# Performance work log

Measured on AMD Instinct MI355X. Metric: run time of the kernel, lower is better.

The kernel has to match this reference:

```python
import jax, jax.numpy as jnp
import numpy as np

EPS = 1e-7
MAX_TAN_NORM = 10.0  # safe_expmap0 clamp


def logmap0(x):
    # x: [..., D] Lorentz point, x[..., 0] = time component (>= 1)
    x0 = x[..., :1]
    xs = x[..., 1:]
    d = jnp.arccosh(jnp.clip(x0, 1.0 + EPS, None))          # geodesic distance to origin
    ns = jnp.clip(jnp.linalg.norm(xs, axis=-1, keepdims=True), EPS, None)
    return jnp.concatenate([jnp.zeros_like(x0), d * xs / ns], axis=-1)


def safe_expmap0(u):
    # u: tangent at origin; time component is projected out (proju at origin)
    us = u[..., 1:]
    n = jnp.clip(jnp.linalg.norm(us, axis=-1, keepdims=True), EPS, None)
    nc = jnp.minimum(n, MAX_TAN_NORM)                        # clamp norm for stability
    usc = us * (nc / n)
    return jnp.concatenate([jnp.cosh(nc), jnp.sinh(nc) * usc / nc], axis=-1)


def projx(x):
    # re-project onto the hyperboloid: x0 = sqrt(1 + ||xs||^2)
    xs = x[..., 1:]
    x0 = jnp.sqrt(1.0 + jnp.sum(xs * xs, axis=-1, keepdims=True))
    return jnp.concatenate([x0, xs], axis=-1)


def lorentz_linear(x_hyp, W, b):
    t = logmap0(x_hyp)
    y = t @ W.T + b
    return projx(safe_expmap0(y))


def setup_inputs() -> dict:
    key = jax.random.key(0)
    ks = jax.random.split(key, 8)
    N, D_IN, D_HID, D_OUT = 8192, 1024, 4096, 1024
    s = 0.02
    x_sp = jax.random.normal(ks[0], (N, D_IN), dtype=jnp.float32)
    x_hyp = projx(x_sp)  # valid Lorentz point (time comp overwritten)
    W1 = jax.random.normal(ks[1], (D_HID, D_IN), dtype=jnp.float32) * s
    b1 = jnp.zeros((D_HID,), dtype=jnp.float32)
    W2 = jax.random.normal(ks[2], (D_HID, D_HID), dtype=jnp.float32) * s
    b2 = jnp.zeros((D_HID,), dtype=jnp.float32)
    W3 = jax.random.normal(ks[3], (D_OUT, D_HID), dtype=jnp.float32) * s
    b3 = jnp.zeros((D_OUT,), dtype=jnp.float32)
    return {"x_hyp": x_hyp, "W1": W1, "b1": b1, "W2": W2, "b2": b2, "W3": W3, "b3": b3}


def reference(x_hyp, W1, b1, W2, b2, W3, b3):
    # layers[:-1] with inter-layer logmap0 -> (dropout=identity in eval) -> expmap0 -> projx
    h = lorentz_linear(x_hyp, W1, b1)
    h = projx(safe_expmap0(logmap0(h)))
    h = lorentz_linear(h, W2, b2)
    h = projx(safe_expmap0(logmap0(h)))
    return lorentz_linear(h, W3, b3)
```

## Files before the change

### kernel.cpp

```cpp
#include <hip/hip_runtime.h>
#include <stdint.h>

#define EPSF 1e-7f
#define MAXTAN 10.0f

typedef __bf16 bf16x8 __attribute__((ext_vector_type(8)));
typedef float floatx4 __attribute__((ext_vector_type(4)));
typedef __attribute__((address_space(3))) void lds_void_t;
typedef __attribute__((address_space(1))) void gbl_void_t;

__device__ __forceinline__ unsigned short f2bf(float x) {
  union { float f; uint32_t u; } v; v.f = x;
  uint32_t u = v.u;
  u += 0x7fffu + ((u >> 16) & 1u);
  return (unsigned short)(u >> 16);
}
__device__ __forceinline__ float bf2f(unsigned short h) {
  union { uint32_t u; float f; } v; v.u = ((uint32_t)h) << 16;
  return v.f;
}

__device__ __forceinline__ int sniff_mode(const unsigned short* x) {
  int sane = 0;
  for (int i = 0; i < 128; ++i) {
    unsigned short h = x[i];
    int e = (h >> 7) & 0xFF;
    if ((h & 0x7FFF) == 0 || (e >= 96 && e <= 140)) ++sane;
  }
  return (sane >= 120) ? 1 : 0;
}

__global__ void k_init(const unsigned short* __restrict__ x, int* __restrict__ modeg,
                       const void* __restrict__ b1, const void* __restrict__ b2,
                       const void* __restrict__ b3, float* __restrict__ o1,
                       float* __restrict__ o2, float* __restrict__ o3) {
  __shared__ int mds;
  if (threadIdx.x == 0) {
    int m = sniff_mode(x);
    mds = m;
    if (blockIdx.x == 0) *modeg = m;
  }
  __syncthreads();
  int m = mds;
  int i = blockIdx.x * 256 + threadIdx.x;
  if (i < 4096) o1[i] = m ? bf2f(((const unsigned short*)b1)[i]) : ((const float*)b1)[i];
  if (i < 4096) o2[i] = m ? bf2f(((const unsigned short*)b2)[i]) : ((const float*)b2)[i];
  if (i < 1024) o3[i] = m ? bf2f(((const unsigned short*)b3)[i]) : ((const float*)b3)[i];
}

__global__ void k_prep(const void* __restrict__ xv, unsigned short* __restrict__ xb,
                       float* __restrict__ sc0, float* __restrict__ x0c,
                       const int* __restrict__ mode) {
  const int row = blockIdx.x;
  const int tid = threadIdx.x;
  float4 v;
  if (*mode) {
    ushort4 u = ((const ushort4*)((const unsigned short*)xv + (size_t)row * 1024))[tid];
    v.x = bf2f(u.x); v.y = bf2f(u.y); v.z = bf2f(u.z); v.w = bf2f(u.w);
  } else {
    v = ((const float4*)((const float*)xv + (size_t)row * 1024))[tid];
  }
  ushort4 o;
  o.x = f2bf(v.x); o.y = f2bf(v.y); o.z = f2bf(v.z); o.w = f2bf(v.w);
  ((ushort4*)(xb + (size_t)row * 1024))[tid] = o;

  float s = v.x * v.x + v.y * v.y + v.z * v.z + v.w * v.w;
  if (tid == 0) s -= v.x * v.x;
  for (int off = 32; off; off >>= 1) s += __shfl_down(s, off, 64);
  __shared__ float red[4];
  if ((tid & 63) == 0) red[tid >> 6] = s;
  __syncthreads();
  if (tid == 0) {
    s = red[0] + red[1] + red[2] + red[3];
    float ns = fmaxf(sqrtf(s), EPSF);
    float d = acoshf(fmaxf(v.x, 1.0f + EPSF));
    sc0[row] = d / ns;
    x0c[row] = bf2f(o.x);
  }
}

template<int K8>
__global__ void k_cvtw(const void* __restrict__ in, unsigned short* __restrict__ out,
                       const int* __restrict__ mode, int n8, float* __restrict__ c0) {
  int i = blockIdx.x * 256 + threadIdx.x;
  if (i >= n8) return;
  if (*mode) {
    uint4 g = ((const uint4*)in)[i];
    ((uint4*)out)[i] = g;
    if (i % K8 == 0) c0[i / K8] = bf2f((unsigned short)(g.x & 0xFFFFu));
  } else {
    float4 a = ((const float4*)in)[2 * i];
    float4 b = ((const float4*)in)[2 * i + 1];
    ushort4 oa, ob;
    oa.x = f2bf(a.x); oa.y = f2bf(a.y); oa.z = f2bf(a.z); oa.w = f2bf(a.w);
    ob.x = f2bf(b.x); ob.y = f2bf(b.y); ob.z = f2bf(b.z); ob.w = f2bf(b.w);
    ((ushort4*)out)[2 * i] = oa;
    ((ushort4*)out)[2 * i + 1] = ob;
    if (i % K8 == 0) c0[i / K8] = bf2f(oa.x);
  }
}

template<int NBLK>
__global__ void k_sc(const float* __restrict__ part, const unsigned short* __restrict__ y,
                     int stride, float* __restrict__ sc, float* __restrict__ c0,
                     float* __restrict__ ssout, int nrows) {
  int i = blockIdx.x * 256 + threadIdx.x;
  if (i >= nrows) return;
  float s = 0.f;
#pragma unroll
  for (int j = 0; j < NBLK; ++j) s += part[(size_t)i * NBLK + j];
  float n = fmaxf(sqrtf(fmaxf(s, 0.f)), EPSF);
  sc[i] = fminf(n, MAXTAN) / n;
  c0[i] = bf2f(y[(size_t)i * stride]);
  if (ssout) ssout[i] = s;
}

__global__ void k_final(const unsigned short* __restrict__ y, const float* __restrict__ ss,
                        void* __restrict__ outv, const int* __restrict__ mode) {
  const int row = blockIdx.x;
  const int tid = threadIdx.x;
  float n = fmaxf(sqrtf(fmaxf(ss[row], 0.f)), EPSF);
  float nc = fminf(n, MAXTAN);
  float a = sinhf(nc) / n;
  ushort4 u = ((const ushort4*)(y + (size_t)row * 1024))[tid];
  float4 o;
  o.x = bf2f(u.x) * a; o.y = bf2f(u.y) * a;
  o.z = bf2f(u.z) * a; o.w = bf2f(u.w) * a;
  if (tid == 0) o.x = coshf(nc);
  if (*mode) {
    ushort4 o16;
    o16.x = f2bf(o.x); o16.y = f2bf(o.y); o16.z = f2bf(o.z); o16.w = f2bf(o.w);
    ((ushort4*)outv)[(size_t)row * 256 + tid] = o16;
  } else {
    ((float4*)outv)[(size_t)row * 256 + tid] = o;
  }
}

template<int N, int K, int NBLK, int GX>
__global__ __launch_bounds__(256, 4) void k_gemm_bt(
    const unsigned short* __restrict__ A,
    const unsigned short* __restrict__ B,
    const float* __restrict__ bias,
    const float* __restrict__ sc,
    const float* __restrict__ c0f,
    const float* __restrict__ wc0,
    unsigned short* __restrict__ Cb,
    float* __restrict__ part)
{
  __shared__ __align__(16) unsigned short As[128 * 32];
  __shared__ __align__(16) unsigned short Bs[128 * 32];

  const int tid  = threadIdx.x;
  const int wave = tid >> 6;
  const int lane = tid & 63;
  const int quad = lane >> 4;
  const int m16  = lane & 15;

  const int j = blockIdx.x & 7;
  const int k = blockIdx.x >> 3;
  int bxi, byi;
  if (GX == 32) {
    bxi = 16 * (j & 1) + (k & 15);
    byi = 16 * (j >> 1) + (k >> 4);
  } else {
    bxi = k & 7;
    byi = 8 * j + (k >> 3);
  }
  const int bm = byi * 128;
  const int bn = bxi * 128;

  const int srow = lane >> 2;
  const int scol = (((lane & 3) ^ ((srow >> 1) & 3)) << 3);

  const int wm = (wave >> 1) << 6;
  const int wn = (wave & 1) << 6;

  const int rsw = ((quad ^ ((m16 >> 1) & 3)) << 3);

  const int c0i = wave * 2;
  const unsigned short* ga0 = A + (size_t)(bm + c0i * 16 + srow) * K + scol;
  const unsigned short* ga1 = ga0 + (size_t)16 * K;
  const unsigned short* gb0 = B + (size_t)(bn + c0i * 16 + srow) * K + scol;
  const unsigned short* gb1 = gb0 + (size_t)16 * K;

  floatx4 acc[4][4];
#pragma unroll
  for (int i = 0; i < 4; ++i)
#pragma unroll
    for (int jj = 0; jj < 4; ++jj)
#pragma unroll
      for (int r = 0; r < 4; ++r) acc[i][jj][r] = 0.0f;

  for (int k0 = 0; k0 < K; k0 += 32) {
    __builtin_amdgcn_global_load_lds((gbl_void_t*)(void*)ga0,
                                     (lds_void_t*)(As + c0i * 512), 16, 0, 0);
    __builtin_amdgcn_global_load_lds((gbl_void_t*)(void*)ga1,
                                     (lds_void_t*)(As + c0i * 512 + 512), 16, 0, 0);
    __builtin_amdgcn_global_load_lds((gbl_void_t*)(void*)gb0,
                                     (lds_void_t*)(Bs + c0i * 512), 16, 0, 0);
    __builtin_amdgcn_global_load_lds((gbl_void_t*)(void*)gb1,
                                     (lds_void_t*)(Bs + c0i * 512 + 512), 16, 0, 0);
    ga0 += 32; ga1 += 32; gb0 += 32; gb1 += 32;
    __syncthreads();

    bf16x8 af[4], bfg[4];
#pragma unroll
    for (int t = 0; t < 4; ++t) {
      af[t]  = *(const bf16x8*)(As + (wm + t * 16 + m16) * 32 + rsw);
      bfg[t] = *(const bf16x8*)(Bs + (wn + t * 16 + m16) * 32 + rsw);
    }
#pragma unroll
    for (int mt = 0; mt < 4; ++mt)
#pragma unroll
      for (int nt = 0; nt < 4; ++nt)
        acc[mt][nt] = __builtin_amdgcn_mfma_f32_16x16x32_bf16(af[mt], bfg[nt], acc[mt][nt], 0, 0, 0);
    __syncthreads();
  }

#pragma unroll
  for (int mt = 0; mt < 4; ++mt) {
#pragma unroll
    for (int r = 0; r < 4; ++r) {
      const int gm = bm + wm + mt * 16 + quad * 4 + r;
      const float scv = sc[gm];
      const float c0v = c0f[gm];
      float sq = 0.f;
#pragma unroll
      for (int nt = 0; nt < 4; ++nt) {
        const int gn = bn + wn + nt * 16 + m16;
        float v = scv * (acc[mt][nt][r] - c0v * wc0[gn]) + bias[gn];
        Cb[(size_t)gm * N + gn] = f2bf(v);
        sq += (gn == 0) ? 0.f : v * v;
      }
      sq += __shfl_xor(sq, 1, 64);
      sq += __shfl_xor(sq, 2, 64);
      sq += __shfl_xor(sq, 4, 64);
      sq += __shfl_xor(sq, 8, 64);
      if (m16 == 0) part[(size_t)gm * NBLK + 2 * bxi + (wave & 1)] = sq;
    }
  }
}

template<int N, int K>
__global__ __launch_bounds__(512, 2) void k_gemm256(
    const unsigned short* __restrict__ A,
    const unsigned short* __restrict__ B,
    const float* __restrict__ bias,
    const float* __restrict__ sc,
    const float* __restrict__ c0f,
    const float* __restrict__ wc0,
    unsigned short* __restrict__ Cb,
    float* __restrict__ part)
{
  static_assert(K % 128 == 0 && K / 32 >= 8, "need NT multiple of 4, >= 8");
  constexpr int NT = K / 32;
  __shared__ __align__(16) unsigned short S[4][2][8192];

  const int tid  = threadIdx.x;
  const int wave = tid >> 6;
  const int lane = tid & 63;
  const int quad = lane >> 4;
  const int m16  = lane & 15;
  const int wr   = wave >> 2;
  const int wc   = wave & 3;

  const int j = blockIdx.x & 7;
  const int k = blockIdx.x >> 3;
  const int bxi = 8 * (j & 1) + (k & 7);
  const int byi = 8 * (j >> 1) + (k >> 3);
  const int bm = byi * 256;
  const int bn = bxi * 256;

  const int gsw8 = (((tid & 3) ^ ((tid >> 3) & 3)) << 3);
  const unsigned short* gAp = A + (size_t)(bm + (tid >> 2)) * K + gsw8;
  const unsigned short* gAq = gAp + (size_t)128 * K;
  const unsigned short* gBp = B + (size_t)(bn + (tid >> 2)) * K + gsw8;
  const unsigned short* gBq = gBp + (size_t)128 * K;
  const int ldw = wave * 1024;

  const int rsw8 = ((quad ^ ((m16 >> 1) & 3)) << 3);
  const int aoffB = ((wr * 128 + m16) * 32 + rsw8) * 2;
  const int boffB = ((wc * 64  + m16) * 32 + rsw8) * 2;
  const char* Sb  = (const char*)&S[0][0][0];
  const char* pA  = Sb + aoffB;
  const char* pA2 = pA + 65536;
  const char* pB  = Sb + 16384 + boffB;
  const char* pB2 = pB + 65536;

  floatx4 acc[8][4];
#pragma unroll
  for (int i = 0; i < 8; ++i)
#pragma unroll
    for (int jj = 0; jj < 4; ++jj)
#pragma unroll
      for (int r = 0; r < 4; ++r) acc[i][jj][r] = 0.0f;

#define GLL(SRC, DST) __builtin_amdgcn_global_load_lds((gbl_void_t*)(void*)(SRC), (lds_void_t*)(DST), 16, 0, 0)
#define ARD(S_, M_) (*(const bf16x8*)(((S_) < 2 ? pA : pA2) + ((S_) * 32768 + (M_) * 1024 - ((S_) < 2 ? 0 : 65536))))
#define BRD(S_, N_) (*(const bf16x8*)(((S_) < 2 ? pB : pB2) + ((S_) * 32768 + (N_) * 1024 - ((S_) < 2 ? 0 : 65536))))
#define STG(T_, OFF) { \
    GLL(gAp + (OFF), (char*)Sb + (T_) * 32768 +         ldw); \
    GLL(gAq + (OFF), (char*)Sb + (T_) * 32768 +  8192 + ldw); \
    GLL(gBp + (OFF), (char*)Sb + (T_) * 32768 + 16384 + ldw); \
    GLL(gBq + (OFF), (char*)Sb + (T_) * 32768 + 24576 + ldw); }

  STG(0, 0) STG(1, 32) STG(2, 64)
  asm volatile("s_waitcnt vmcnt(4)" ::: "memory");
  __builtin_amdgcn_s_barrier();

  bf16x8 bX[4], bY[4];
#pragma unroll
  for (int n = 0; n < 4; ++n) bX[n] = BRD(0, n);

#define MBODY(BI, BC, BN)                                                              \
  {                                                                                    \
    STG((BI + 3) & 3, (BI + 3) * 32)                                                   \
    bf16x8 a_[8];                                                                      \
    _Pragma("unroll")                                                                  \
    for (int m = 0; m < 8; ++m) a_[m] = ARD(BI, m);                                    \
    __builtin_amdgcn_s_setprio(1);                                                     \
    _Pragma("unroll")                                                                  \
    for (int f = 0; f < 4; ++f)                                                        \
      _Pragma("unroll")                                                                \
      for (int n = 0; n < 4; ++n)                                                      \
        acc[f][n] = __builtin_amdgcn_mfma_f32_16x16x32_bf16(a_[f], BC[n], acc[f][n], 0, 0, 0); \
    __builtin_amdgcn_s_setprio(0);                                                     \
    _Pragma("unroll")                                                                  \
    for (int n = 0; n < 4; ++n) BN[n] = BRD((BI + 1) & 3, n);                          \
    __builtin_amdgcn_s_setprio(1);                                                     \
    _Pragma("unroll")                                                                  \
    for (int f = 0; f < 4; ++f)                                                        \
      _Pragma("unroll")                                                                \
      for (int n = 0; n < 4; ++n)                                                      \
        acc[f + 4][n] = __builtin_amdgcn_mfma_f32_16x16x32_bf16(a_[f + 4], BC[n], acc[f + 4][n], 0, 0, 0); \
    __builtin_amdgcn_s_setprio(0);                                                     \
    asm volatile("s_waitcnt vmcnt(4)" ::: "memory");                                   \
    __builtin_amdgcn_s_barrier();                                                      \
  }

#define TBODY(BI, BC)                                                                  \
  {                                                                                    \
    bf16x8 a_[8];                                                                      \
    _Pragma("unroll")                                                                  \
    for (int m = 0; m < 8; ++m) a_[m] = ARD(BI, m);                                    \
    __builtin_amdgcn_s_setprio(1);                                                     \
    _Pragma("unroll")                                                                  \
    for (int f = 0; f < 4; ++f)                                                        \
      _Pragma("unroll")                                                                \
      for (int n = 0; n < 4; ++n)                                                      \
        acc[f][n] = __builtin_amdgcn_mfma_f32_16x16x32_bf16(a_[f], BC[n], acc[f][n], 0, 0, 0); \
    _Pragma("unroll")                                                                  \
    for (int f = 0; f < 4; ++f)                                                        \
      _Pragma("unroll")                                                                \
      for (int n = 0; n < 4; ++n)                                                      \
        acc[f + 4][n] = __builtin_amdgcn_mfma_f32_16x16x32_bf16(a_[f + 4], BC[n], acc[f + 4][n], 0, 0, 0); \
    __builtin_amdgcn_s_setprio(0);                                                     \
  }

  for (int t = 0; t < NT - 4; t += 4) {
    MBODY(0, bX, bY)
    MBODY(1, bY, bX)
    MBODY(2, bX, bY)
    MBODY(3, bY, bX)
    gAp += 128; gAq += 128; gBp += 128; gBq += 128;
  }

  STG(3, 96)
  {
    bf16x8 a_[8];
#pragma unroll
    for (int m = 0; m < 8; ++m) a_[m] = ARD(0, m);
    __builtin_amdgcn_s_setprio(1);
#pragma unroll
    for (int f = 0; f < 4; ++f)
#pragma unroll
      for (int n = 0; n < 4; ++n)
        acc[f][n] = __builtin_amdgcn_mfma_f32_16x16x32_bf16(a_[f], bX[n], acc[f][n], 0, 0, 0);
    __builtin_amdgcn_s_setprio(0);
#pragma unroll
    for (int n = 0; n < 4; ++n) bY[n] = BRD(1, n);
    __builtin_amdgcn_s_setprio(1);
#pragma unroll
    for (int f = 0; f < 4; ++f)
#pragma unroll
      for (int n = 0; n < 4; ++n)
        acc[f + 4][n] = __builtin_amdgcn_mfma_f32_16x16x32_bf16(a_[f + 4], bX[n], acc[f + 4][n], 0, 0, 0);
    __builtin_amdgcn_s_setprio(0);
  }
  asm volatile("s_waitcnt vmcnt(0)" ::: "memory");
  __builtin_amdgcn_s_barrier();
  {
    bf16x8 a_[8];
#pragma unroll
    for (int m = 0; m < 8; ++m) a_[m] = ARD(1, m);
    __builtin_amdgcn_s_setprio(1);
#pragma unroll
    for (int f = 0; f < 4; ++f)
#pragma unroll
      for (int n = 0; n < 4; ++n)
        acc[f][n] = __builtin_amdgcn_mfma_f32_16x16x32_bf16(a_[f], bY[n], acc[f][n], 0, 0, 0);
    __builtin_amdgcn_s_setprio(0);
#pragma unroll
    for (int n = 0; n < 4; ++n) bX[n] = BRD(2, n);
    __builtin_amdgcn_s_setprio(1);
#pragma unroll
    for (int f = 0; f < 4; ++f)
#pragma unroll
      for (int n = 0; n < 4; ++n)
        acc[f + 4][n] = __builtin_amdgcn_mfma_f32_16x16x32_bf16(a_[f + 4], bY[n], acc[f + 4][n], 0, 0, 0);
    __builtin_amdgcn_s_setprio(0);
  }
  {
    bf16x8 a_[8];
#pragma unroll
    for (int m = 0; m < 8; ++m) a_[m] = ARD(2, m);
    __builtin_amdgcn_s_setprio(1);
#pragma unroll
    for (int f = 0; f < 4; ++f)
#pragma unroll
      for (int n = 0; n < 4; ++n)
        acc[f][n] = __builtin_amdgcn_mfma_f32_16x16x32_bf16(a_[f], bX[n], acc[f][n], 0, 0, 0);
    __builtin_amdgcn_s_setprio(0);
#pragma unroll
    for (int n = 0; n < 4; ++n) bY[n] = BRD(3, n);
    __builtin_amdgcn_s_setprio(1);
#pragma unroll
    for (int f = 0; f < 4; ++f)
#pragma unroll
      for (int n = 0; n < 4; ++n)
        acc[f + 4][n] = __builtin_amdgcn_mfma_f32_16x16x32_bf16(a_[f + 4], bX[n], acc[f + 4][n], 0, 0, 0);
    __builtin_amdgcn_s_setprio(0);
  }
  TBODY(3, bY)

#undef TBODY
#undef MBODY
#undef STG
#undef BRD
#undef ARD
#undef GLL

  const int wm = wr * 128;
  const int wn = wc * 64;
#pragma unroll
  for (int mt = 0; mt < 8; ++mt) {
#pragma unroll
    for (int r = 0; r < 4; ++r) {
      const int gm = bm + wm + mt * 16 + quad * 4 + r;
      const float scv = sc[gm];
      const float c0v = c0f[gm];
      float sq = 0.f;
#pragma unroll
      for (int nt = 0; nt < 4; ++nt) {
        const int gn = bn + wn + nt * 16 + m16;
        float v = scv * (acc[mt][nt][r] - c0v * wc0[gn]) + bias[gn];
        Cb[(size_t)gm * N + gn] = f2bf(v);
        sq += (gn == 0) ? 0.f : v * v;
      }
      sq += __shfl_xor(sq, 1, 64);
      sq += __shfl_xor(sq, 2, 64);
      sq += __shfl_xor(sq, 4, 64);
      sq += __shfl_xor(sq, 8, 64);
      if (m16 == 0) part[(size_t)gm * 64 + bxi * 4 + wc] = sq;
    }
  }
}

extern "C" void kernel_launch(void* const* d_in, const int* in_sizes, int n_in,
                              void* d_out, int out_size, void* d_ws, size_t ws_size,
                              hipStream_t stream) {
  const void* x  = d_in[0];
  const void* W1 = d_in[1];
  const void* b1 = d_in[2];
  const void* W2 = d_in[3];
  const void* b2 = d_in[4];
  const void* W3 = d_in[5];
  const void* b3 = d_in[6];

  const int NR = 8192, DIN = 1024, DH = 4096, DOUT = 1024;

  char* ws = (char*)d_ws;
  size_t off = 0;
  int* mode = (int*)(ws + off);                        off += 256;
  unsigned short* W1b = (unsigned short*)(ws + off);   off += (size_t)DH * DIN * 2;
  unsigned short* W2b = (unsigned short*)(ws + off);   off += (size_t)DH * DH * 2;
  unsigned short* W3b = (unsigned short*)(ws + off);   off += (size_t)DOUT * DH * 2;
  unsigned short* xb  = (unsigned short*)(ws + off);   off += (size_t)NR * DIN * 2;
  unsigned short* y1  = (unsigned short*)(ws + off);   off += (size_t)NR * DH * 2;
  unsigned short* y2  = (unsigned short*)(ws + off);   off += (size_t)NR * DH * 2;
  unsigned short* y3  = (unsigned short*)(ws + off);   off += (size_t)NR * DOUT * 2;
  float* part1 = (float*)(ws + off);                   off += (size_t)NR * 64 * 4;
  float* part2 = (float*)(ws + off);                   off += (size_t)NR * 64 * 4;
  float* part3 = (float*)(ws + off);                   off += (size_t)NR * 16 * 4;
  float* sc0  = (float*)(ws + off);                    off += (size_t)NR * 4;
  float* x0c  = (float*)(ws + off);                    off += (size_t)NR * 4;
  float* sc1  = (float*)(ws + off);                    off += (size_t)NR * 4;
  float* c01  = (float*)(ws + off);                    off += (size_t)NR * 4;
  float* sc2  = (float*)(ws + off);                    off += (size_t)NR * 4;
  float* c02  = (float*)(ws + off);                    off += (size_t)NR * 4;
  float* ss3  = (float*)(ws + off);                    off += (size_t)NR * 4;
  float* w1c0 = (float*)(ws + off);                    off += (size_t)DH * 4;
  float* w2c0 = (float*)(ws + off);                    off += (size_t)DH * 4;
  float* w3c0 = (float*)(ws + off);                    off += (size_t)DOUT * 4;
  float* b1f  = (float*)(ws + off);                    off += (size_t)DH * 4;
  float* b2f  = (float*)(ws + off);                    off += (size_t)DH * 4;
  float* b3f  = (float*)(ws + off);                    off += (size_t)DOUT * 4;

  k_init<<<16, 256, 0, stream>>>((const unsigned short*)x, mode, b1, b2, b3, b1f, b2f, b3f);

  k_cvtw<128><<<(DH * DIN / 8 + 255) / 256, 256, 0, stream>>>(W1, W1b, mode, DH * DIN / 8, w1c0);
  k_cvtw<512><<<(DH * DH  / 8 + 255) / 256, 256, 0, stream>>>(W2, W2b, mode, DH * DH / 8, w2c0);
  k_cvtw<512><<<(DOUT * DH / 8 + 255) / 256, 256, 0, stream>>>(W3, W3b, mode, DOUT * DH / 8, w3c0);

  k_prep<<<NR, 256, 0, stream>>>(x, xb, sc0, x0c, mode);

  k_gemm256<4096, 1024><<<512, 512, 0, stream>>>(
      xb, W1b, b1f, sc0, x0c, w1c0, y1, part1);
  k_sc<64><<<(NR + 255) / 256, 256, 0, stream>>>(part1, y1, DH, sc1, c01, nullptr, NR);

  k_gemm256<4096, 4096><<<512, 512, 0, stream>>>(
      y1, W2b, b2f, sc1, c01, w2c0, y2, part2);
  k_sc<64><<<(NR + 255) / 256, 256, 0, stream>>>(part2, y2, DH, sc2, c02, nullptr, NR);

  k_gemm_bt<1024, 4096, 16, 8><<<512, 256, 0, stream>>>(
      y2, W3b, b3f, sc2, c02, w3c0, y3, part3);
  k_sc<16><<<(NR + 255) / 256, 256, 0, stream>>>(part3, y3, DOUT, sc0, x0c, ss3, NR);

  k_final<<<NR, 256, 0, stream>>>(y3, ss3, d_out, mode);
}
```

Measured before the change: 594.1 us.

## Load B fragments directly from global into registers, bypass LDS for B

The GEMM kernel no longer stages the B (weight) tile through shared memory. Each wave loads its B fragments straight from global memory into registers one k-step ahead, while only A is staged through LDS. This halves LDS usage (which could raise occupancy) and removes the LDS reads for B. In exchange, B is re-read from global/L2 by each of the two wave rows, and the loads are uncoalesced 16-byte per-lane row reads whose latency must be hidden by the one-step register prefetch.

```diff
diff --git a/kernel.cpp b/kernel.cpp
--- a/kernel.cpp
+++ b/kernel.cpp
@@ -254,7 +254,7 @@
 {
   static_assert(K % 128 == 0 && K / 32 >= 8, "need NT multiple of 4, >= 8");
   constexpr int NT = K / 32;
-  __shared__ __align__(16) unsigned short S[4][2][8192];
+  __shared__ __align__(16) unsigned short S[4][8192];
 
   const int tid  = threadIdx.x;
   const int wave = tid >> 6;
@@ -274,18 +274,16 @@
   const int gsw8 = (((tid & 3) ^ ((tid >> 3) & 3)) << 3);
   const unsigned short* gAp = A + (size_t)(bm + (tid >> 2)) * K + gsw8;
   const unsigned short* gAq = gAp + (size_t)128 * K;
-  const unsigned short* gBp = B + (size_t)(bn + (tid >> 2)) * K + gsw8;
-  const unsigned short* gBq = gBp + (size_t)128 * K;
+  char* SbW = (char*)&S[0][0];
   const int ldw = wave * 1024;
 
+  const unsigned short* pB0 = B + (size_t)(bn + wc * 64 + m16) * K + quad * 8;
+  const unsigned short* pB1 = pB0 + (size_t)16 * K;
+  const unsigned short* pB2 = pB0 + (size_t)32 * K;
+  const unsigned short* pB3 = pB0 + (size_t)48 * K;
+
   const int rsw8 = ((quad ^ ((m16 >> 1) & 3)) << 3);
-  const int aoffB = ((wr * 128 + m16) * 32 + rsw8) * 2;
-  const int boffB = ((wc * 64  + m16) * 32 + rsw8) * 2;
-  const char* Sb  = (const char*)&S[0][0][0];
-  const char* pA  = Sb + aoffB;
-  const char* pA2 = pA + 65536;
-  const char* pB  = Sb + 16384 + boffB;
-  const char* pB2 = pB + 65536;
+  const char* Ab = (const char*)&S[0][0] + ((wr * 128 + m16) * 32 + rsw8) * 2;
 
   floatx4 acc[8][4];
 #pragma unroll
@@ -296,65 +294,36 @@
       for (int r = 0; r < 4; ++r) acc[i][jj][r] = 0.0f;
 
 #define GLL(SRC, DST) __builtin_amdgcn_global_load_lds((gbl_void_t*)(void*)(SRC), (lds_void_t*)(DST), 16, 0, 0)
-#define ARD(S_, M_) (*(const bf16x8*)(((S_) < 2 ? pA : pA2) + ((S_) * 32768 + (M_) * 1024 - ((S_) < 2 ? 0 : 65536))))
-#define BRD(S_, N_) (*(const bf16x8*)(((S_) < 2 ? pB : pB2) + ((S_) * 32768 + (N_) * 1024 - ((S_) < 2 ? 0 : 65536))))
-#define STG(T_, OFF) { \
-    GLL(gAp + (OFF), (char*)Sb + (T_) * 32768 +         ldw); \
-    GLL(gAq + (OFF), (char*)Sb + (T_) * 32768 +  8192 + ldw); \
-    GLL(gBp + (OFF), (char*)Sb + (T_) * 32768 + 16384 + ldw); \
-    GLL(gBq + (OFF), (char*)Sb + (T_) * 32768 + 24576 + ldw); }
-
+#define STG(SL, CO) { GLL(gAp + (CO), SbW + (SL) * 16384 + ldw); \
+                      GLL(gAq + (CO), SbW + (SL) * 16384 + 8192 + ldw); }
+#define LDB(BN, CO) { BN[0] = *(const bf16x8*)(pB0 + (CO)); \
+                      BN[1] = *(const bf16x8*)(pB1 + (CO)); \
+                      BN[2] = *(const bf16x8*)(pB2 + (CO)); \
+                      BN[3] = *(const bf16x8*)(pB3 + (CO)); }
+#define ARD(SL, M_) (*(const bf16x8*)(Ab + (SL) * 16384 + (M_) * 1024))
+
+  bf16x8 bX[4], bY[4];
+  LDB(bX, 0)
   STG(0, 0) STG(1, 32) STG(2, 64)
   asm volatile("s_waitcnt vmcnt(4)" ::: "memory");
   __builtin_amdgcn_s_barrier();
 
-  bf16x8 bX[4], bY[4];
-#pragma unroll
-  for (int n = 0; n < 4; ++n) bX[n] = BRD(0, n);
-
 #define MBODY(BI, BC, BN)                                                              \
   {                                                                                    \
+    LDB(BN, (BI + 1) * 32)                                                             \
     STG((BI + 3) & 3, (BI + 3) * 32)                                                   \
     bf16x8 a_[8];                                                                      \
     _Pragma("unroll")                                                                  \
     for (int m = 0; m < 8; ++m) a_[m] = ARD(BI, m);                                    \
     __builtin_amdgcn_s_setprio(1);                                                     \
     _Pragma("unroll")                                                                  \
-    for (int f = 0; f < 4; ++f)                                                        \
+    for (int f = 0; f < 8; ++f)                                                        \
       _Pragma("unroll")                                                                \
       for (int n = 0; n < 4; ++n)                                                      \
         acc[f][n] = __builtin_amdgcn_mfma_f32_16x16x32_bf16(a_[f], BC[n], acc[f][n], 0, 0, 0); \
     __builtin_amdgcn_s_setprio(0);                                                     \
-    _Pragma("unroll")                                                                  \
-    for (int n = 0; n < 4; ++n) BN[n] = BRD((BI + 1) & 3, n);                          \
-    __builtin_amdgcn_s_setprio(1);                                                     \
-    _Pragma("unroll")                                                                  \
-    for (int f = 0; f < 4; ++f)                                                        \
-      _Pragma("unroll")                                                                \
-      for (int n = 0; n < 4; ++n)                                                      \
-        acc[f + 4][n] = __builtin_amdgcn_mfma_f32_16x16x32_bf16(a_[f + 4], BC[n], acc[f + 4][n], 0, 0, 0); \
-    __builtin_amdgcn_s_setprio(0);                                                     \
-    asm volatile("s_waitcnt vmcnt(4)" ::: "memory");                                   \
+    asm volatile("s_waitcnt vmcnt(2)" ::: "memory");                                   \
     __builtin_amdgcn_s_barrier();                                                      \
-  }
-
-#define TBODY(BI, BC)                                                                  \
-  {                                                                                    \
-    bf16x8 a_[8];                                                                      \
-    _Pragma("unroll")                                                                  \
-    for (int m = 0; m < 8; ++m) a_[m] = ARD(BI, m);                                    \
-    __builtin_amdgcn_s_setprio(1);                                                     \
-    _Pragma("unroll")                                                                  \
-    for (int f = 0; f < 4; ++f)                                                        \
-      _Pragma("unroll")                                                                \
-      for (int n = 0; n < 4; ++n)                                                      \
-        acc[f][n] = __builtin_amdgcn_mfma_f32_16x16x32_bf16(a_[f], BC[n], acc[f][n], 0, 0, 0); \
-    _Pragma("unroll")                                                                  \
-    for (int f = 0; f < 4; ++f)                                                        \
-      _Pragma("unroll")                                                                \
-      for (int n = 0; n < 4; ++n)                                                      \
-        acc[f + 4][n] = __builtin_amdgcn_mfma_f32_16x16x32_bf16(a_[f + 4], BC[n], acc[f + 4][n], 0, 0, 0); \
-    __builtin_amdgcn_s_setprio(0);                                                     \
   }
 
   for (int t = 0; t < NT - 4; t += 4) {
@@ -362,82 +331,68 @@
     MBODY(1, bY, bX)
     MBODY(2, bX, bY)
     MBODY(3, bY, bX)
-    gAp += 128; gAq += 128; gBp += 128; gBq += 128;
+    gAp += 128; gAq += 128; pB0 += 128; pB1 += 128; pB2 += 128; pB3 += 128;
   }
 
   STG(3, 96)
   {
+    LDB(bY, 32)
     bf16x8 a_[8];
 #pragma unroll
     for (int m = 0; m < 8; ++m) a_[m] = ARD(0, m);
     __builtin_amdgcn_s_setprio(1);
 #pragma unroll
-    for (int f = 0; f < 4; ++f)
+    for (int f = 0; f < 8; ++f)
 #pragma unroll
       for (int n = 0; n < 4; ++n)
         acc[f][n] = __builtin_amdgcn_mfma_f32_16x16x32_bf16(a_[f], bX[n], acc[f][n], 0, 0, 0);
     __builtin_amdgcn_s_setprio(0);
-#pragma unroll
-    for (int n = 0; n < 4; ++n) bY[n] = BRD(1, n);
-    __builtin_amdgcn_s_setprio(1);
-#pragma unroll
-    for (int f = 0; f < 4; ++f)
-#pragma unroll
-      for (int n = 0; n < 4; ++n)
-        acc[f + 4][n] = __builtin_amdgcn_mfma_f32_16x16x32_bf16(a_[f + 4], bX[n], acc[f + 4][n], 0, 0, 0);
-    __builtin_amdgcn_s_setprio(0);
   }
   asm volatile("s_waitcnt vmcnt(0)" ::: "memory");
   __builtin_amdgcn_s_barrier();
   {
+    LDB(bX, 64)
     bf16x8 a_[8];
 #pragma unroll
     for (int m = 0; m < 8; ++m) a_[m] = ARD(1, m);
     __builtin_amdgcn_s_setprio(1);
 #pragma unroll
-    for (int f = 0; f < 4; ++f)
+    for (int f = 0; f < 8; ++f)
 #pragma unroll
       for (int n = 0; n < 4; ++n)
         acc[f][n] = __builtin_amdgcn_mfma_f32_16x16x32_bf16(a_[f], bY[n], acc[f][n], 0, 0, 0);
     __builtin_amdgcn_s_setprio(0);
-#pragma unroll
-    for (int n = 0; n < 4; ++n) bX[n] = BRD(2, n);
-    __builtin_amdgcn_s_setprio(1);
-#pragma unroll
-    for (int f = 0; f < 4; ++f)
-#pragma unroll
-      for (int n = 0; n < 4; ++n)
-        acc[f + 4][n] = __builtin_amdgcn_mfma_f32_16x16x32_bf16(a_[f + 4], bY[n], acc[f + 4][n], 0, 0, 0);
-    __builtin_amdgcn_s_setprio(0);
   }
   {
+    LDB(bY, 96)
     bf16x8 a_[8];
 #pragma unroll
     for (int m = 0; m < 8; ++m) a_[m] = ARD(2, m);
     __builtin_amdgcn_s_setprio(1);
 #pragma unroll
-    for (int f = 0; f < 4; ++f)
+    for (int f = 0; f < 8; ++f)
 #pragma unroll
       for (int n = 0; n < 4; ++n)
         acc[f][n] = __builtin_amdgcn_mfma_f32_16x16x32_bf16(a_[f], bX[n], acc[f][n], 0, 0, 0);
     __builtin_amdgcn_s_setprio(0);
-#pragma unroll
-    for (int n = 0; n < 4; ++n) bY[n] = BRD(3, n);
+  }
+  {
+    bf16x8 a_[8];
+#pragma unroll
+    for (int m = 0; m < 8; ++m) a_[m] = ARD(3, m);
     __builtin_amdgcn_s_setprio(1);
 #pragma unroll
-    for (int f = 0; f < 4; ++f)
+    for (int f = 0; f < 8; ++f)
 #pragma unroll
       for (int n = 0; n < 4; ++n)
-        acc[f + 4][n] = __builtin_amdgcn_mfma_f32_16x16x32_bf16(a_[f + 4], bX[n], acc[f + 4][n], 0, 0, 0);
+        acc[f][n] = __builtin_amdgcn_mfma_f32_16x16x32_bf16(a_[f], bY[n], acc[f][n], 0, 0, 0);
     __builtin_amdgcn_s_setprio(0);
   }
-  TBODY(3, bY)
-
-#undef TBODY
+
 #undef MBODY
+#undef ARD
+#undef LDB
 #undef STG
-#undef BRD
-#undef ARD
 #undef GLL
 
   const int wm = wr * 128;
```

Measured after the change: 734.6 us. 1.24x slower.
